# Performance work log

Measured on AMD Instinct MI355X. Metric: run time of the kernel, lower is better.

The kernel has to match this reference:

```python
import jax, jax.numpy as jnp
import numpy as np

INIT_STDEV = 0.01

def setup_inputs() -> dict:
    key = jax.random.key(0)
    k1, k2, k3 = jax.random.split(key, 3)
    B, S, D = 8, 4096, 768
    x = jax.random.normal(k1, (B, S, D), dtype=jnp.float32)
    att_v = jax.random.normal(k2, (D,), dtype=jnp.float32) * INIT_STDEV
    att_W = jax.random.normal(k3, (D, D), dtype=jnp.float32) * INIT_STDEV
    return {"x": x, "att_v": att_v, "att_W": att_W}

def reference(x, att_v, att_W):
    # y = x @ W : [B,S,D]; scores = tanh(y) . v over D : [B,S]
    y = jnp.tanh(jnp.einsum('bsd,de->bse', x, att_W))
    scores = jnp.einsum('bsd,d->bs', y, att_v)
    weights = jax.nn.softmax(scores, axis=-1)            # softmax over sequence
    out = jnp.einsum('bs,bsd->bd', weights, x)           # attsum pool
    return out.astype(jnp.float32)
```

## Files before the change

### kernel.cpp

```cpp
#include <hip/hip_runtime.h>
#include <hip/hip_bf16.h>

constexpr int Bb = 8;
constexpr int Ss = 4096;
constexpr int Dd = 768;
constexpr int Mm = Bb * Ss;

typedef __bf16 bf16x8 __attribute__((ext_vector_type(8)));
typedef float f32x4 __attribute__((ext_vector_type(4)));

__device__ __forceinline__ float fast_tanh(float x) {
    return 1.f - 2.f / (__expf(2.f * x) + 1.f);
}

__device__ __forceinline__ void load_lds16(const void* g, void* l) {
    __builtin_amdgcn_global_load_lds(
        (const __attribute__((address_space(1))) unsigned int*)g,
        (__attribute__((address_space(3))) unsigned int*)l, 16, 0, 0);
}

__global__ __launch_bounds__(256) void convW(const float* __restrict__ W,
                                             __bf16* __restrict__ Wt) {
    __shared__ float tile[32][33];
    const int tx = threadIdx.x & 31;
    const int ty = threadIdx.x >> 5;
    const int kb = blockIdx.x * 32;
    const int nb = blockIdx.y * 32;
#pragma unroll
    for (int i = 0; i < 32; i += 8)
        tile[ty + i][tx] = W[(size_t)(kb + ty + i) * Dd + nb + tx];
    __syncthreads();
#pragma unroll
    for (int i = 0; i < 32; i += 8) {
        const int n = nb + ty + i;
        const int txs = (tx & 7) | ((((tx >> 3) & 3) ^ ((n >> 1) & 3)) << 3);
        Wt[(size_t)n * Dd + kb + txs] = (__bf16)tile[tx][ty + i];
    }
}

__global__ __launch_bounds__(512, 4) void scores_gemm(
    const float* __restrict__ x, const __bf16* __restrict__ Wt,
    const float* __restrict__ v, float* __restrict__ scores3) {
    __shared__ float  As[2][128 * 32];
    __shared__ __bf16 Bs[3][256 * 32];

    const int t = threadIdx.x;
    const int id = blockIdx.x;
    const int ids = ((id & 7) * 96) + (id >> 3);
    const int mb = ids / 3;
    const int nb = ids - mb * 3;
    const int lane = t & 63;
    const int wave = t >> 6;
    const int wm = wave >> 2;
    const int wn = wave & 3;
    const int quad = lane >> 4;
    const int lid = lane & 15;
    const int rslot = ((quad ^ ((lid >> 1) & 3)) * 8);

    const int sarow = t >> 3;
    const int sarot = ((sarow & 1) << 2) | ((sarow >> 1) & 3);
    const int sacoll = (t & 7) ^ sarot;
    const float* axp = x + (size_t)(mb * 128 + sarow) * Dd + sacoll * 4;
    const float* axp1 = axp + (size_t)64 * Dd;

    const __bf16* bg[3];
    int bl[3];
#pragma unroll
    for (int j = 0; j < 3; ++j) {
        const int flat = j * 8192 / 3 * 3;
        (void)flat;
        const int f2 = j * 8192 + t * 16;
        (void)f2;
        bg[j] = nullptr; bl[j] = 0;
    }
    const __bf16* bgp[2];
    int blp[2];
#pragma unroll
    for (int j = 0; j < 2; ++j) {
        const int flat = j * 8192 + t * 16;
        const int col = flat >> 6;
        bgp[j] = Wt + (size_t)(nb * 256 + col) * Dd + ((flat & 63) >> 1);
        blp[j] = flat >> 1;
    }

    const int arot = ((lid & 1) << 2) | ((lid >> 1) & 3);
    const int s0 = ((2 * quad) ^ arot) * 4;
    const int s1 = ((2 * quad + 1) ^ arot) * 4;

    f32x4 acc[4][4];
#pragma unroll
    for (int tm = 0; tm < 4; ++tm)
#pragma unroll
        for (int nt = 0; nt < 4; ++nt) acc[tm][nt] = (f32x4){0.f, 0.f, 0.f, 0.f};

    load_lds16(axp, &As[0][t * 4]);
    load_lds16(axp1, &As[0][2048 + t * 4]);
#pragma unroll
    for (int j = 0; j < 2; ++j) load_lds16(bgp[j], &Bs[0][blp[j]]);
#pragma unroll
    for (int j = 0; j < 2; ++j) load_lds16(bgp[j] + 32, &Bs[1][blp[j]]);

#pragma unroll
    for (int k = 0; k < 24; ++k) {
        if (k == 23) asm volatile("s_waitcnt vmcnt(0)" ::: "memory");
        else         asm volatile("s_waitcnt vmcnt(2)" ::: "memory");
        __builtin_amdgcn_sched_barrier(0);
        __builtin_amdgcn_s_barrier();
        __builtin_amdgcn_sched_barrier(0);

        if (k < 23) {
            load_lds16(axp + (k + 1) * 32, &As[(k + 1) & 1][t * 4]);
            load_lds16(axp1 + (k + 1) * 32, &As[(k + 1) & 1][2048 + t * 4]);
        }
        if (k < 22) {
#pragma unroll
            for (int j = 0; j < 2; ++j)
                load_lds16(bgp[j] + (k + 2) * 32, &Bs[(k + 2) % 3][blp[j]]);
        }
        __builtin_amdgcn_sched_barrier(0);

        bf16x8 af[4], bfr[4];
#pragma unroll
        for (int tm = 0; tm < 4; ++tm) {
            const int rowb = (wm * 64 + tm * 16 + lid) * 32;
            const f32x4 lo = *(const f32x4*)(&As[k & 1][rowb + s0]);
            const f32x4 hi = *(const f32x4*)(&As[k & 1][rowb + s1]);
            bf16x8 a;
            a[0] = (__bf16)lo[0]; a[1] = (__bf16)lo[1];
            a[2] = (__bf16)lo[2]; a[3] = (__bf16)lo[3];
            a[4] = (__bf16)hi[0]; a[5] = (__bf16)hi[1];
            a[6] = (__bf16)hi[2]; a[7] = (__bf16)hi[3];
            af[tm] = a;
        }
#pragma unroll
        for (int nt = 0; nt < 4; ++nt)
            bfr[nt] = *(const bf16x8*)(&Bs[k % 3][(wn * 64 + nt * 16 + lid) * 32 + rslot]);

        __builtin_amdgcn_s_setprio(1);
#pragma unroll
        for (int tm = 0; tm < 4; ++tm)
#pragma unroll
            for (int nt = 0; nt < 4; ++nt)
                acc[tm][nt] = __builtin_amdgcn_mfma_f32_16x16x32_bf16(af[tm], bfr[nt], acc[tm][nt], 0, 0, 0);
        __builtin_amdgcn_s_setprio(0);
    }

    __syncthreads();
    float* ssc = (float*)&As[0][0];

    float vv[4];
#pragma unroll
    for (int nt = 0; nt < 4; ++nt)
        vv[nt] = v[nb * 256 + wn * 64 + nt * 16 + lid];

#pragma unroll
    for (int tm = 0; tm < 4; ++tm)
#pragma unroll
        for (int r = 0; r < 4; ++r) {
            float s = 0.f;
#pragma unroll
            for (int nt = 0; nt < 4; ++nt) s += vv[nt] * fast_tanh(acc[tm][nt][r]);
            s += __shfl_xor(s, 1);
            s += __shfl_xor(s, 2);
            s += __shfl_xor(s, 4);
            s += __shfl_xor(s, 8);
            if (lid == 0) ssc[wave * 64 + tm * 16 + quad * 4 + r] = s;
        }
    __syncthreads();
    if (t < 128) {
        const int wmh = t >> 6;
        const int rl = t & 63;
        float s = 0.f;
#pragma unroll
        for (int ww = 0; ww < 4; ++ww) s += ssc[(wmh * 4 + ww) * 64 + rl];
        scores3[(size_t)nb * Mm + mb * 128 + t] = s;
    }
}

__global__ __launch_bounds__(256) void softmax_k(const float* __restrict__ scores3,
                                                 float* __restrict__ weights,
                                                 float* __restrict__ sinv) {
    const int b = blockIdx.x;
    const int t = threadIdx.x;
    const float* s0 = scores3 + (size_t)b * Ss;
    const float* s1 = s0 + Mm;
    const float* s2 = s1 + Mm;
    float* wgt = weights + (size_t)b * Ss;
    __shared__ float red[256];

    float mx = -1e30f;
    for (int i = t; i < Ss; i += 256) {
        const float sc = s0[i] + s1[i] + s2[i];
        wgt[i] = sc;
        mx = fmaxf(mx, sc);
    }
    red[t] = mx;
    __syncthreads();
    for (int o = 128; o > 0; o >>= 1) {
        if (t < o) red[t] = fmaxf(red[t], red[t + o]);
        __syncthreads();
    }
    mx = red[0];
    __syncthreads();
    float sum = 0.f;
    for (int i = t; i < Ss; i += 256) {
        const float e = __expf(wgt[i] - mx);
        wgt[i] = e;
        sum += e;
    }
    red[t] = sum;
    __syncthreads();
    for (int o = 128; o > 0; o >>= 1) {
        if (t < o) red[t] += red[t + o];
        __syncthreads();
    }
    if (t == 0) sinv[b] = 1.f / red[0];
}

__global__ __launch_bounds__(192) void pool1(const float* __restrict__ x,
                                             const float* __restrict__ weights,
                                             float* __restrict__ partial) {
    const int b = blockIdx.y;
    const int c = blockIdx.x;
    const int t = threadIdx.x;
    const float* base = x + ((size_t)b * Ss + c * 32) * Dd;
    const float* wrow = weights + (size_t)b * Ss + c * 32;
    float4 acc = make_float4(0.f, 0.f, 0.f, 0.f);
#pragma unroll 8
    for (int i = 0; i < 32; ++i) {
        const float ww = wrow[i];
        const float4 xv = *(const float4*)(base + (size_t)i * Dd + t * 4);
        acc.x += ww * xv.x;
        acc.y += ww * xv.y;
        acc.z += ww * xv.z;
        acc.w += ww * xv.w;
    }
    *(float4*)(partial + ((size_t)(b * 128 + c)) * Dd + t * 4) = acc;
}

__global__ __launch_bounds__(768) void pool2(const float* __restrict__ partial,
                                             const float* __restrict__ sinv,
                                             float* __restrict__ out) {
    const int b = blockIdx.x;
    const int d = threadIdx.x;
    float s = 0.f;
#pragma unroll 8
    for (int c = 0; c < 128; ++c) s += partial[((size_t)(b * 128 + c)) * Dd + d];
    out[(size_t)b * Dd + d] = s * sinv[b];
}

extern "C" void kernel_launch(void* const* d_in, const int* in_sizes, int n_in,
                              void* d_out, int out_size, void* d_ws, size_t ws_size,
                              hipStream_t stream) {
    (void)in_sizes; (void)n_in; (void)ws_size; (void)out_size;
    const float* x = (const float*)d_in[0];
    const float* v = (const float*)d_in[1];
    const float* W = (const float*)d_in[2];

    char* ws = (char*)d_ws;
    __bf16* Wt = (__bf16*)ws;
    float* scores3 = (float*)(ws + 1179648);
    float* weights = (float*)(ws + 1179648 + 393216);
    float* sinv    = (float*)(ws + 1179648 + 393216 + 131072);
    float* partial = (float*)(ws + 1179648 + 393216 + 131072 + 32);

    convW<<<dim3(Dd / 32, Dd / 32), 256, 0, stream>>>(W, Wt);
    scores_gemm<<<dim3(3 * Mm / 128), 512, 0, stream>>>(x, Wt, v, scores3);
    softmax_k<<<dim3(Bb), 256, 0, stream>>>(scores3, weights, sinv);
    pool1<<<dim3(128, Bb), 192, 0, stream>>>(x, weights, partial);
    pool2<<<dim3(Bb), 768, 0, stream>>>(partial, sinv, (float*)d_out);
}
```

Baseline: 245.7 us.

## Rework A-tile LDS layout in scores GEMM and widen pool2 grid

Changes the A-tile staging in the scores GEMM. Each row's 32 floats are now split into two 16-float halves stored in separate LDS regions, with a simple XOR swizzle, in place of the previous row-rotation swizzle. The aim is to make global_load_lds writes and MFMA fragment reads more contiguous and lower LDS bank conflicts. The pool2 reduction is spread over 6x8 blocks of 128 threads instead of 8 blocks of 768, for more parallelism. The score scratch now lives in Bs, and the partial buffer is offset to 128-byte alignment.

```diff
diff --git a/kernel.cpp b/kernel.cpp
--- a/kernel.cpp
+++ b/kernel.cpp
@@ -41,7 +41,7 @@
 __global__ __launch_bounds__(512, 4) void scores_gemm(
     const float* __restrict__ x, const __bf16* __restrict__ Wt,
     const float* __restrict__ v, float* __restrict__ scores3) {
-    __shared__ float  As[2][128 * 32];
+    __shared__ float  As[2][4096];
     __shared__ __bf16 Bs[3][256 * 32];
 
     const int t = threadIdx.x;
@@ -57,22 +57,10 @@
     const int lid = lane & 15;
     const int rslot = ((quad ^ ((lid >> 1) & 3)) * 8);
 
-    const int sarow = t >> 3;
-    const int sarot = ((sarow & 1) << 2) | ((sarow >> 1) & 3);
-    const int sacoll = (t & 7) ^ sarot;
-    const float* axp = x + (size_t)(mb * 128 + sarow) * Dd + sacoll * 4;
-    const float* axp1 = axp + (size_t)64 * Dd;
-
-    const __bf16* bg[3];
-    int bl[3];
-#pragma unroll
-    for (int j = 0; j < 3; ++j) {
-        const int flat = j * 8192 / 3 * 3;
-        (void)flat;
-        const int f2 = j * 8192 + t * 16;
-        (void)f2;
-        bg[j] = nullptr; bl[j] = 0;
-    }
+    const int sarow = t >> 2;
+    const float* axg0 = x + (size_t)(mb * 128 + sarow) * Dd + (t & 3) * 4;
+    const float* axg1 = x + (size_t)(mb * 128 + sarow) * Dd + 16 + (((t & 3) ^ 1) * 4);
+
     const __bf16* bgp[2];
     int blp[2];
 #pragma unroll
@@ -83,9 +71,11 @@
         blp[j] = flat >> 1;
     }
 
-    const int arot = ((lid & 1) << 2) | ((lid >> 1) & 3);
-    const int s0 = ((2 * quad) ^ arot) * 4;
-    const int s1 = ((2 * quad + 1) ^ arot) * 4;
+    const int p_ = quad >> 1;
+    const int sA0 = ((quad & 1) * 2 + 0) ^ p_;
+    const int sA1 = ((quad & 1) * 2 + 1) ^ p_;
+    const int abase = p_ * 2048 + sA0 * 4;
+    const int abase1 = p_ * 2048 + sA1 * 4;
 
     f32x4 acc[4][4];
 #pragma unroll
@@ -93,8 +83,8 @@
 #pragma unroll
         for (int nt = 0; nt < 4; ++nt) acc[tm][nt] = (f32x4){0.f, 0.f, 0.f, 0.f};
 
-    load_lds16(axp, &As[0][t * 4]);
-    load_lds16(axp1, &As[0][2048 + t * 4]);
+    load_lds16(axg0, &As[0][t * 4]);
+    load_lds16(axg1, &As[0][2048 + t * 4]);
 #pragma unroll
     for (int j = 0; j < 2; ++j) load_lds16(bgp[j], &Bs[0][blp[j]]);
 #pragma unroll
@@ -109,8 +99,8 @@
         __builtin_amdgcn_sched_barrier(0);
 
         if (k < 23) {
-            load_lds16(axp + (k + 1) * 32, &As[(k + 1) & 1][t * 4]);
-            load_lds16(axp1 + (k + 1) * 32, &As[(k + 1) & 1][2048 + t * 4]);
+            load_lds16(axg0 + (k + 1) * 32, &As[(k + 1) & 1][t * 4]);
+            load_lds16(axg1 + (k + 1) * 32, &As[(k + 1) & 1][2048 + t * 4]);
         }
         if (k < 22) {
 #pragma unroll
@@ -122,14 +112,14 @@
         bf16x8 af[4], bfr[4];
 #pragma unroll
         for (int tm = 0; tm < 4; ++tm) {
-            const int rowb = (wm * 64 + tm * 16 + lid) * 32;
-            const f32x4 lo = *(const f32x4*)(&As[k & 1][rowb + s0]);
-            const f32x4 hi = *(const f32x4*)(&As[k & 1][rowb + s1]);
+            const int row = wm * 64 + tm * 16 + lid;
+            const f32x4 r1 = *(const f32x4*)(&As[k & 1][abase + row * 16]);
+            const f32x4 r2 = *(const f32x4*)(&As[k & 1][abase1 + row * 16]);
             bf16x8 a;
-            a[0] = (__bf16)lo[0]; a[1] = (__bf16)lo[1];
-            a[2] = (__bf16)lo[2]; a[3] = (__bf16)lo[3];
-            a[4] = (__bf16)hi[0]; a[5] = (__bf16)hi[1];
-            a[6] = (__bf16)hi[2]; a[7] = (__bf16)hi[3];
+            a[0] = (__bf16)r1[0]; a[1] = (__bf16)r1[1];
+            a[2] = (__bf16)r1[2]; a[3] = (__bf16)r1[3];
+            a[4] = (__bf16)r2[0]; a[5] = (__bf16)r2[1];
+            a[6] = (__bf16)r2[2]; a[7] = (__bf16)r2[3];
             af[tm] = a;
         }
 #pragma unroll
@@ -146,7 +136,7 @@
     }
 
     __syncthreads();
-    float* ssc = (float*)&As[0][0];
+    float* ssc = (float*)&Bs[0][0];
 
     float vv[4];
 #pragma unroll
@@ -238,11 +228,11 @@
     *(float4*)(partial + ((size_t)(b * 128 + c)) * Dd + t * 4) = acc;
 }
 
-__global__ __launch_bounds__(768) void pool2(const float* __restrict__ partial,
+__global__ __launch_bounds__(128) void pool2(const float* __restrict__ partial,
                                              const float* __restrict__ sinv,
                                              float* __restrict__ out) {
-    const int b = blockIdx.x;
-    const int d = threadIdx.x;
+    const int b = blockIdx.y;
+    const int d = blockIdx.x * 128 + threadIdx.x;
     float s = 0.f;
 #pragma unroll 8
     for (int c = 0; c < 128; ++c) s += partial[((size_t)(b * 128 + c)) * Dd + d];
@@ -258,15 +248,21 @@
     const float* W = (const float*)d_in[2];
 
     char* ws = (char*)d_ws;
-    __bf16* Wt = (__bf16*)ws;
-    float* scores3 = (float*)(ws + 1179648);
-    float* weights = (float*)(ws + 1179648 + 393216);
-    float* sinv    = (float*)(ws + 1179648 + 393216 + 131072);
-    float* partial = (float*)(ws + 1179648 + 393216 + 131072 + 32);
+    constexpr size_t OFF_WT = 0;
+    constexpr size_t OFF_SC = 1179648;
+    constexpr size_t OFF_WG = OFF_SC + 393216;
+    constexpr size_t OFF_SI = OFF_WG + 131072;
+    constexpr size_t OFF_PA = OFF_SI + 128;
+
+    __bf16* Wt     = (__bf16*)(ws + OFF_WT);
+    float* scores3 = (float*)(ws + OFF_SC);
+    float* weights = (float*)(ws + OFF_WG);
+    float* sinv    = (float*)(ws + OFF_SI);
+    float* partial = (float*)(ws + OFF_PA);
 
     convW<<<dim3(Dd / 32, Dd / 32), 256, 0, stream>>>(W, Wt);
     scores_gemm<<<dim3(3 * Mm / 128), 512, 0, stream>>>(x, Wt, v, scores3);
     softmax_k<<<dim3(Bb), 256, 0, stream>>>(scores3, weights, sinv);
     pool1<<<dim3(128, Bb), 192, 0, stream>>>(x, weights, partial);
-    pool2<<<dim3(Bb), 768, 0, stream>>>(partial, sinv, (float*)d_out);
-}
+    pool2<<<dim3(6, Bb), 128, 0, stream>>>(partial, sinv, (float*)d_out);
+}
```

New measurement: 242.6 us. No clear change (-1.3%).
